# Kernel tuning notes

Hardware: AMD Instinct MI355X
Metric: run time of the kernel (lower is better)

Reference implementation:

```python
import jax, jax.numpy as jnp
import numpy as np

EMBED_DIM = 1024
NUM_HEADS = 16
TGT_LEN = 2048
SRC_LEN = 2048
BSZ = 8
SCALING = float(EMBED_DIM // NUM_HEADS) ** (-0.5)


def setup_inputs() -> dict:
    key = jax.random.key(0)
    k1, k2, k3, k4 = jax.random.split(key, 4)
    q1 = jax.random.normal(k1, (TGT_LEN, BSZ, EMBED_DIM), dtype=jnp.float32)
    k = jax.random.normal(k2, (SRC_LEN, BSZ, EMBED_DIM), dtype=jnp.float32)
    value = jax.random.normal(k3, (SRC_LEN, BSZ, EMBED_DIM), dtype=jnp.float32)
    # nn.Linear weight [out, in], xavier-ish scale
    W = jax.random.normal(k4, (EMBED_DIM, EMBED_DIM), dtype=jnp.float32) / np.sqrt(EMBED_DIM)
    b = jnp.zeros((EMBED_DIM,), dtype=jnp.float32)
    return {"q1": q1, "k": k, "value": value, "W": W, "b": b}


def reference(q1, k, value, W, b):
    # q1: [T, B, E], k: [S, B, E]; `value` is unused (module projects v from k).
    del value
    v = k @ W.T + b                      # [S, B, E] fused v-projection
    q = (q1 * SCALING).transpose(1, 0, 2)  # [B, T, E]
    kt = k.transpose(1, 0, 2)              # [B, S, E]
    vt = v.transpose(1, 0, 2)              # [B, S, E]
    scores = jnp.einsum('bte,bse->bts', q, kt)   # [B, T, S]
    attn = jax.nn.softmax(scores, axis=-1)
    out = jnp.einsum('bts,bse->bte', attn, vt)   # [B, T, E]
    return out.transpose(1, 0, 2)                # [T, B, E]
```

## Files before the change

kernel.cpp:

```cpp
#include <hip/hip_runtime.h>
#include <hip/hip_bf16.h>

#define E_DIM 1024
#define T_LEN 2048
#define S_LEN 2048
#define B_SZ  8
#define SCALE 0.125f

typedef short short8 __attribute__((ext_vector_type(8)));
typedef float f32x4 __attribute__((ext_vector_type(4)));

#define BARRIER() __builtin_amdgcn_s_barrier()

static __device__ __forceinline__ unsigned short f2bf(float f) {
  __hip_bfloat16 h = __float2bfloat16(f);
  return __builtin_bit_cast(unsigned short, h);
}

__global__ __launch_bounds__(256) void prep_kernel(
    const float* __restrict__ q1, const float* __restrict__ kin,
    const float* __restrict__ W,
    unsigned short* __restrict__ qbf, unsigned short* __restrict__ kbf,
    unsigned short* __restrict__ wbf, float* __restrict__ denom) {
  const int QV = B_SZ * T_LEN * (E_DIM / 4);
  const int WV = (E_DIM * E_DIM) / 4;
  const int DN = (B_SZ * T_LEN) / 4;
  const int total = 2 * QV + WV + DN;
  for (int idx = blockIdx.x * blockDim.x + threadIdx.x; idx < total;
       idx += gridDim.x * blockDim.x) {
    if (idx < QV) {
      int e4 = idx & 255;
      int bt = idx >> 8;
      int t = bt & (T_LEN - 1);
      int b = bt >> 11;
      float4 v = reinterpret_cast<const float4*>(q1)[(t * B_SZ + b) * 256 + e4];
      ushort4 o;
      o.x = f2bf(v.x * SCALE); o.y = f2bf(v.y * SCALE);
      o.z = f2bf(v.z * SCALE); o.w = f2bf(v.w * SCALE);
      reinterpret_cast<ushort4*>(qbf)[idx] = o;
    } else if (idx < 2 * QV) {
      int d = idx - QV;
      int e4 = d & 255;
      int bt = d >> 8;
      int s = bt & (T_LEN - 1);
      int b = bt >> 11;
      float4 v = reinterpret_cast<const float4*>(kin)[(s * B_SZ + b) * 256 + e4];
      ushort4 o;
      o.x = f2bf(v.x); o.y = f2bf(v.y); o.z = f2bf(v.z); o.w = f2bf(v.w);
      reinterpret_cast<ushort4*>(kbf)[d] = o;
    } else if (idx < 2 * QV + WV) {
      int d = idx - 2 * QV;
      float4 v = reinterpret_cast<const float4*>(W)[d];
      ushort4 o;
      o.x = f2bf(v.x); o.y = f2bf(v.y); o.z = f2bf(v.z); o.w = f2bf(v.w);
      reinterpret_cast<ushort4*>(wbf)[d] = o;
    } else {
      int d = idx - 2 * QV - WV;
      float4 z; z.x = z.y = z.z = z.w = 0.f;
      reinterpret_cast<float4*>(denom)[d] = z;
    }
  }
}

#define RD(ptr, off) (*reinterpret_cast<const short8*>((ptr) + (off)))

#define STAGE(srcs, dstBase, KOFF)                                            \
  {                                                                           \
    _Pragma("unroll") for (int p_ = 0; p_ < 2; ++p_) {                        \
      unsigned short* dst_ = (dstBase) + (size_t)(p_ * 512 + wave * 64) * 8;  \
      __builtin_amdgcn_global_load_lds(                                       \
          (const __attribute__((address_space(1))) unsigned int*)             \
              ((srcs)[p_] + (KOFF)),                                          \
          (__attribute__((address_space(3))) unsigned int*)dst_, 16, 0, 0);   \
    }                                                                         \
  }

#define MFMAQ(MB, NB, AF, BF)                                                 \
  {                                                                           \
    _Pragma("unroll") for (int m_ = 0; m_ < 4; ++m_)                          \
      _Pragma("unroll") for (int n_ = 0; n_ < 2; ++n_)                        \
        _Pragma("unroll") for (int ks_ = 0; ks_ < 2; ++ks_)                   \
          acc[MB + m_][NB + n_] = __builtin_amdgcn_mfma_f32_16x16x32_bf16(    \
              AF[m_][ks_], BF[n_][ks_], acc[MB + m_][NB + n_], 0, 0, 0);      \
  }

#define LGKM0() asm volatile("s_waitcnt lgkmcnt(0)" ::: "memory")

#define KTILE(S, DO_B, DO_A, KOB, KOA)                                        \
  {                                                                           \
    short8 aL[4][2], aH[4][2], bb[2][2];                                      \
            \
    _Pragma("unroll") for (int m = 0; m < 4; ++m) {                           \
      aL[m][0] = RD(pA0, S * 16384 + m * 1024);                               \
      aL[m][1] = RD(pA1, S * 16384 + m * 1024);                               \
    }                                                                         \
    _Pragma("unroll") for (int n = 0; n < 2; ++n) {                           \
      bb[n][0] = RD(pB0, S * 16384 + n * 1024);                               \
      bb[n][1] = RD(pB1, S * 16384 + n * 1024);                               \
    }                                                                         \
    if (DO_B) STAGE(sB0, ldsB + (1 - S) * 16384, KOB);                        \
    BARRIER();                                                                \
    __builtin_amdgcn_s_setprio(1);                                            \
    MFMAQ(0, 0, aL, bb);                                                      \
    __builtin_amdgcn_s_setprio(0);                                            \
    LGKM0();                                                                  \
    BARRIER();                                                                \
                      \
    _Pragma("unroll") for (int m = 0; m < 4; ++m) {                           \
      aH[m][0] = RD(pA0, S * 16384 + (4 + m) * 1024);                         \
      aH[m][1] = RD(pA1, S * 16384 + (4 + m) * 1024);                         \
    }                                                                         \
    if (DO_B) STAGE(sB1, ldsB + (1 - S) * 16384 + 8192, KOB);                 \
    BARRIER();                                                                \
    __builtin_amdgcn_s_setprio(1);                                            \
    MFMAQ(4, 0, aH, bb);                                                      \
    __builtin_amdgcn_s_setprio(0);                                            \
    LGKM0();                                                                  \
    BARRIER();                                                                \
                     \
    _Pragma("unroll") for (int n = 0; n < 2; ++n) {                           \
      bb[n][0] = RD(pB0, S * 16384 + (2 + n) * 1024);                         \
      bb[n][1] = RD(pB1, S * 16384 + (2 + n) * 1024);                         \
    }                                                                         \
    if (DO_A) STAGE(sA0, ldsA + S * 16384, KOA);                              \
    BARRIER();                                                                \
    __builtin_amdgcn_s_setprio(1);                                            \
    MFMAQ(0, 2, aL, bb);                                                      \
    __builtin_amdgcn_s_setprio(0);                                            \
    LGKM0();                                                                  \
    BARRIER();                                                                \
                     \
    if (DO_A) {                                                               \
      STAGE(sA1, ldsA + S * 16384 + 8192, KOA);                               \
      asm volatile("s_waitcnt vmcnt(4)" ::: "memory");                        \
    } else {                                                                  \
      asm volatile("s_waitcnt vmcnt(0)" ::: "memory");                        \
    }                                                                         \
    BARRIER();                                                                \
    __builtin_amdgcn_s_setprio(1);                                            \
    MFMAQ(4, 2, aH, bb);                                                      \
    __builtin_amdgcn_s_setprio(0);                                            \
    LGKM0();                                                                  \
    BARRIER();                                                                \
  }

__device__ __forceinline__ void gemm256(
    const unsigned short* __restrict__ A, size_t lda, int r0,
    const unsigned short* __restrict__ B, size_t ldb, int c0,
    int NKT, unsigned short* lds, f32x4 acc[8][4]) {
  const int tid = threadIdx.x;
  const int lane = tid & 63, wave = tid >> 6;
  const int lr = lane & 15, lg = lane >> 4;
  const int wr = wave >> 2, wc = wave & 3;
  unsigned short* ldsA = lds;
  unsigned short* ldsB = lds + 4 * 8192;

  const unsigned short* pA0 = ldsA + wr * 8192 + lr * 64 + ((0 + lg) ^ (lr & 7)) * 8;
  const unsigned short* pA1 = ldsA + wr * 8192 + lr * 64 + ((4 + lg) ^ (lr & 7)) * 8;
  const unsigned short* pB0 = ldsB + (wc >> 1) * 8192 + ((wc & 1) * 64 + lr) * 64 +
                              ((0 + lg) ^ (lr & 7)) * 8;
  const unsigned short* pB1 = ldsB + (wc >> 1) * 8192 + ((wc & 1) * 64 + lr) * 64 +
                              ((4 + lg) ^ (lr & 7)) * 8;

  const unsigned short* sA0[2]; const unsigned short* sA1[2];
  const unsigned short* sB0[2]; const unsigned short* sB1[2];
#pragma unroll
  for (int p = 0; p < 2; ++p) {
    int c = p * 512 + tid, row = c >> 3, cg = (c & 7) ^ (row & 7);
    sA0[p] = A + (size_t)(r0 + row) * lda + cg * 8;
    sA1[p] = A + (size_t)(r0 + 128 + row) * lda + cg * 8;
    sB0[p] = B + (size_t)(c0 + row) * ldb + cg * 8;
    sB1[p] = B + (size_t)(c0 + 128 + row) * ldb + cg * 8;
  }

  STAGE(sA0, ldsA, 0);
  STAGE(sA1, ldsA + 8192, 0);
  STAGE(sB0, ldsB, 0);
  STAGE(sB1, ldsB + 8192, 0);
  STAGE(sA0, ldsA + 16384, 64);
  STAGE(sA1, ldsA + 16384 + 8192, 64);
  asm volatile("s_waitcnt vmcnt(4)" ::: "memory");
  BARRIER();

  const int nit = NKT >> 1;
  for (int it = 0; it < nit; ++it) {
    const bool notLast = (it != nit - 1);
    KTILE(0, true, notLast, 64, 128);
    KTILE(1, notLast, notLast, 128, 192);
#pragma unroll
    for (int p = 0; p < 2; ++p) {
      sA0[p] += 128; sA1[p] += 128; sB0[p] += 128; sB1[p] += 128;
    }
  }
}

__global__ __launch_bounds__(512, 2) void proj_kernel(
    const unsigned short* __restrict__ kbf,
    const unsigned short* __restrict__ wbf,
    const float* __restrict__ bias,
    unsigned short* __restrict__ vT) {
  __shared__ unsigned short lds[65536];
  const int lane = threadIdx.x & 63, wave = threadIdx.x >> 6;
  const int lr = lane & 15, lg = lane >> 4;
  const int wr = wave >> 2, wc = wave & 3;
  const int r0 = blockIdx.x * 256;
  const int c0 = blockIdx.y * 256;
  f32x4 acc[8][4] = {};
  gemm256(kbf, E_DIM, r0, wbf, E_DIM, c0, E_DIM / 64, lds, acc);
#pragma unroll
  for (int n = 0; n < 4; ++n) {
    int o = c0 + wc * 64 + n * 16 + lr;
    float bv = bias[o];
#pragma unroll
    for (int m = 0; m < 8; ++m) {
#pragma unroll
      for (int i = 0; i < 4; ++i) {
        int r = r0 + wr * 128 + m * 16 + lg * 4 + i;
        int b = r >> 11;
        int s = r & (S_LEN - 1);
        vT[((size_t)b * E_DIM + o) * S_LEN + s] = f2bf(acc[m][n][i] + bv);
      }
    }
  }
}

__global__ __launch_bounds__(512, 2) void scores_kernel(
    const unsigned short* __restrict__ qbf,
    const unsigned short* __restrict__ kbf,
    unsigned short* __restrict__ P, float* __restrict__ denom,
    int tbase, int trows, int ntx) {
  __shared__ unsigned short lds[65536];
  const int nwg = gridDim.x;
  const int per = nwg >> 3;
  const int wgid = (blockIdx.x & 7) * per + (blockIdx.x >> 3);
  const int b = wgid / (ntx * 8);
  const int rem = wgid - b * (ntx * 8);
  const int ty = rem / ntx;
  const int tx = rem - ty * ntx;
  const int lane = threadIdx.x & 63, wave = threadIdx.x >> 6;
  const int lr = lane & 15, lg = lane >> 4;
  const int wr = wave >> 2, wc = wave & 3;
  const int t0l = tx * 256;
  const int s0 = ty * 256;
  const unsigned short* Q = qbf + (size_t)b * T_LEN * E_DIM;
  const unsigned short* K = kbf + (size_t)b * S_LEN * E_DIM;
  f32x4 acc[8][4] = {};
  gemm256(Q, E_DIM, tbase + t0l, K, E_DIM, s0, E_DIM / 64, lds, acc);
  unsigned short* outp = P + (size_t)b * trows * S_LEN;
  float* dn = denom + (size_t)b * T_LEN + tbase;
#pragma unroll
  for (int m = 0; m < 8; ++m) {
#pragma unroll
    for (int i = 0; i < 4; ++i) {
      int tl = t0l + wr * 128 + m * 16 + lg * 4 + i;
      float rp = 0.f;
#pragma unroll
      for (int n = 0; n < 4; ++n) {
        float e = __expf(acc[m][n][i]);
        rp += e;
        int s = s0 + wc * 64 + n * 16 + lr;
        outp[(size_t)tl * S_LEN + s] = f2bf(e);
      }
#pragma unroll
      for (int off = 1; off < 16; off <<= 1) rp += __shfl_xor(rp, off);
      if (lr == 0) atomicAdd(&dn[tl], rp);
    }
  }
}

__global__ __launch_bounds__(512, 2) void pv_kernel(
    const unsigned short* __restrict__ pbf,
    const unsigned short* __restrict__ vT,
    const float* __restrict__ denom,
    float* __restrict__ out, int tbase, int trows, int ntx) {
  __shared__ unsigned short lds[65536];
  const int nwg = gridDim.x;
  const int per = nwg >> 3;
  const int wgid = (blockIdx.x & 7) * per + (blockIdx.x >> 3);
  const int b = wgid / (ntx * 4);
  const int rem = wgid - b * (ntx * 4);
  const int ey = rem / ntx;
  const int tx = rem - ey * ntx;
  const int lane = threadIdx.x & 63, wave = threadIdx.x >> 6;
  const int lr = lane & 15, lg = lane >> 4;
  const int wr = wave >> 2, wc = wave & 3;
  const int tl0 = tx * 256;
  const int e0 = ey * 256;
  const unsigned short* Pp = pbf + (size_t)b * trows * S_LEN;
  const unsigned short* V = vT + (size_t)b * E_DIM * S_LEN;
  f32x4 acc[8][4] = {};
  gemm256(Pp, S_LEN, tl0, V, S_LEN, e0, S_LEN / 64, lds, acc);
  const float* dn = denom + (size_t)b * T_LEN + tbase;
#pragma unroll
  for (int m = 0; m < 8; ++m) {
#pragma unroll
    for (int i = 0; i < 4; ++i) {
      int tl = tl0 + wr * 128 + m * 16 + lg * 4 + i;
      float invd = 1.0f / dn[tl];
      int t = tbase + tl;
#pragma unroll
      for (int n = 0; n < 4; ++n) {
        int e = e0 + wc * 64 + n * 16 + lr;
        out[((size_t)t * B_SZ + b) * E_DIM + e] = acc[m][n][i] * invd;
      }
    }
  }
}

extern "C" void kernel_launch(void* const* d_in, const int* in_sizes, int n_in,
                              void* d_out, int out_size, void* d_ws, size_t ws_size,
                              hipStream_t stream) {
  const float* q1 = (const float*)d_in[0];
  const float* k = (const float*)d_in[1];
  const float* W = (const float*)d_in[3];
  const float* bias = (const float*)d_in[4];
  float* out = (float*)d_out;

  char* ws = (char*)d_ws;
  const size_t QB = (size_t)B_SZ * T_LEN * E_DIM * 2;
  const size_t WBYTES = (size_t)E_DIM * E_DIM * 2;
  const size_t DBYTES = (size_t)B_SZ * T_LEN * 4;
  unsigned short* qbf = (unsigned short*)(ws);
  unsigned short* kbf = (unsigned short*)(ws + QB);
  unsigned short* vT = (unsigned short*)(ws + 2 * QB);
  unsigned short* wbf = (unsigned short*)(ws + 3 * QB);
  float* denom = (float*)(ws + 3 * QB + WBYTES);
  unsigned short* P = (unsigned short*)(ws + 3 * QB + WBYTES + DBYTES);
  const size_t fixed = 3 * QB + WBYTES + DBYTES;

  size_t avail = ws_size > fixed ? ws_size - fixed : 0;
  int tpc = (int)(avail / ((size_t)B_SZ * S_LEN * 2));
  tpc = (tpc / 256) * 256;
  if (tpc > T_LEN) tpc = T_LEN;
  if (tpc < 256) tpc = 256;

  prep_kernel<<<dim3(2048), dim3(256), 0, stream>>>(q1, k, W, qbf, kbf, wbf,
                                                    denom);
  proj_kernel<<<dim3((B_SZ * S_LEN) / 256, E_DIM / 256), dim3(512), 0, stream>>>(
      kbf, wbf, bias, vT);

  for (int tbase = 0; tbase < T_LEN; tbase += tpc) {
    int trows = T_LEN - tbase < tpc ? T_LEN - tbase : tpc;
    int ntx = trows / 256;
    scores_kernel<<<dim3(ntx * (S_LEN / 256) * B_SZ), dim3(512), 0, stream>>>(
        qbf, kbf, P, denom, tbase, trows, ntx);
    pv_kernel<<<dim3(ntx * (E_DIM / 256) * B_SZ), dim3(512), 0, stream>>>(
        P, vT, denom, out, tbase, trows, ntx);
  }
}
```

Measured before the change: 220.3 us.

## Software-pipeline LDS fragment reads across MFMA phases and drop explicit lgkmcnt waits

```diff
diff --git a/kernel.cpp b/kernel.cpp
--- a/kernel.cpp
+++ b/kernel.cpp
@@ -84,64 +84,56 @@
               AF[m_][ks_], BF[n_][ks_], acc[MB + m_][NB + n_], 0, 0, 0);      \
   }
 
-#define LGKM0() asm volatile("s_waitcnt lgkmcnt(0)" ::: "memory")
-
 #define KTILE(S, DO_B, DO_A, KOB, KOA)                                        \
   {                                                                           \
-    short8 aL[4][2], aH[4][2], bb[2][2];                                      \
-            \
-    _Pragma("unroll") for (int m = 0; m < 4; ++m) {                           \
-      aL[m][0] = RD(pA0, S * 16384 + m * 1024);                               \
-      aL[m][1] = RD(pA1, S * 16384 + m * 1024);                               \
-    }                                                                         \
-    _Pragma("unroll") for (int n = 0; n < 2; ++n) {                           \
-      bb[n][0] = RD(pB0, S * 16384 + n * 1024);                               \
-      bb[n][1] = RD(pB1, S * 16384 + n * 1024);                               \
-    }                                                                         \
+           \
     if (DO_B) STAGE(sB0, ldsB + (1 - S) * 16384, KOB);                        \
-    BARRIER();                                                                \
-    __builtin_amdgcn_s_setprio(1);                                            \
-    MFMAQ(0, 0, aL, bb);                                                      \
-    __builtin_amdgcn_s_setprio(0);                                            \
-    LGKM0();                                                                  \
-    BARRIER();                                                                \
-                      \
     _Pragma("unroll") for (int m = 0; m < 4; ++m) {                           \
       aH[m][0] = RD(pA0, S * 16384 + (4 + m) * 1024);                         \
       aH[m][1] = RD(pA1, S * 16384 + (4 + m) * 1024);                         \
     }                                                                         \
+    __builtin_amdgcn_s_setprio(1);                                            \
+    MFMAQ(0, 0, aL, b01);                                                     \
+    __builtin_amdgcn_s_setprio(0);                                            \
+    BARRIER();                                                        \
+          \
     if (DO_B) STAGE(sB1, ldsB + (1 - S) * 16384 + 8192, KOB);                 \
-    BARRIER();                                                                \
+    _Pragma("unroll") for (int n = 0; n < 2; ++n) {                           \
+      b23[n][0] = RD(pB0, S * 16384 + (2 + n) * 1024);                        \
+      b23[n][1] = RD(pB1, S * 16384 + (2 + n) * 1024);                        \
+    }                                                                         \
     __builtin_amdgcn_s_setprio(1);                                            \
-    MFMAQ(4, 0, aH, bb);                                                      \
+    MFMAQ(4, 0, aH, b01);                                                     \
     __builtin_amdgcn_s_setprio(0);                                            \
-    LGKM0();                                                                  \
-    BARRIER();                                                                \
-                     \
-    _Pragma("unroll") for (int n = 0; n < 2; ++n) {                           \
-      bb[n][0] = RD(pB0, S * 16384 + (2 + n) * 1024);                         \
-      bb[n][1] = RD(pB1, S * 16384 + (2 + n) * 1024);                         \
-    }                                                                         \
+    BARRIER();                                                        \
+                    \
     if (DO_A) STAGE(sA0, ldsA + S * 16384, KOA);                              \
-    BARRIER();                                                                \
     __builtin_amdgcn_s_setprio(1);                                            \
-    MFMAQ(0, 2, aL, bb);                                                      \
+    MFMAQ(0, 2, aL, b23);                                                     \
     __builtin_amdgcn_s_setprio(0);                                            \
-    LGKM0();                                                                  \
-    BARRIER();                                                                \
-                     \
+    BARRIER();                                                        \
+     \
     if (DO_A) {                                                               \
       STAGE(sA1, ldsA + S * 16384 + 8192, KOA);                               \
       asm volatile("s_waitcnt vmcnt(4)" ::: "memory");                        \
     } else {                                                                  \
       asm volatile("s_waitcnt vmcnt(0)" ::: "memory");                        \
     }                                                                         \
-    BARRIER();                                                                \
+    BARRIER();                     \
+    if (DO_B) {                                                               \
+      _Pragma("unroll") for (int m = 0; m < 4; ++m) {                         \
+        aL[m][0] = RD(pA0, (1 - S) * 16384 + m * 1024);                       \
+        aL[m][1] = RD(pA1, (1 - S) * 16384 + m * 1024);                       \
+      }                                                                       \
+      _Pragma("unroll") for (int n = 0; n < 2; ++n) {                         \
+        b01[n][0] = RD(pB0, (1 - S) * 16384 + n * 1024);                      \
+        b01[n][1] = RD(pB1, (1 - S) * 16384 + n * 1024);                      \
+      }                                                                       \
+    }                                                                         \
     __builtin_amdgcn_s_setprio(1);                                            \
-    MFMAQ(4, 2, aH, bb);                                                      \
+    MFMAQ(4, 2, aH, b23);                                                     \
     __builtin_amdgcn_s_setprio(0);                                            \
-    LGKM0();                                                                  \
-    BARRIER();                                                                \
+    BARRIER();                                        \
   }
 
 __device__ __forceinline__ void gemm256(
@@ -173,6 +165,8 @@
     sB1[p] = B + (size_t)(c0 + 128 + row) * ldb + cg * 8;
   }
 
+  short8 aL[4][2], aH[4][2], b01[2][2], b23[2][2];
+
   STAGE(sA0, ldsA, 0);
   STAGE(sA1, ldsA + 8192, 0);
   STAGE(sB0, ldsB, 0);
@@ -181,6 +175,16 @@
   STAGE(sA1, ldsA + 16384 + 8192, 64);
   asm volatile("s_waitcnt vmcnt(4)" ::: "memory");
   BARRIER();
+#pragma unroll
+  for (int m = 0; m < 4; ++m) {
+    aL[m][0] = RD(pA0, m * 1024);
+    aL[m][1] = RD(pA1, m * 1024);
+  }
+#pragma unroll
+  for (int n = 0; n < 2; ++n) {
+    b01[n][0] = RD(pB0, n * 1024);
+    b01[n][1] = RD(pB1, n * 1024);
+  }
 
   const int nit = NKT >> 1;
   for (int it = 0; it < nit; ++it) {
```

New measurement: 272.8 us. 23.8% more time.
